# Optimization experiments

Measured on AMD Instinct MI355X. Metric: run time of the kernel, lower is better.

## Reference

```python
import jax, jax.numpy as jnp
import numpy as np

B, TQ, TI, TT = 8, 256, 256, 256
H, NH, F, E = 1024, 16, 4096, 8
HD = H // NH
EPS = 1e-5


def _ln(x, g, b):
    m = x.mean(-1, keepdims=True)
    v = ((x - m) ** 2).mean(-1, keepdims=True)
    return (x - m) / jnp.sqrt(v + EPS) * g + b


def _mha(q, k, v, in_w, in_b, out_w, out_b):
    # torch nn.MultiheadAttention: packed in_proj [3H,H], out_proj [H,H]
    wq, wk, wv = jnp.split(in_w, 3, axis=0)
    bq, bk, bv = jnp.split(in_b, 3, axis=0)
    Bq, Tq, _ = q.shape
    Tk = k.shape[1]
    qh = (q @ wq.T + bq).reshape(Bq, Tq, NH, HD)
    kh = (k @ wk.T + bk).reshape(Bq, Tk, NH, HD)
    vh = (v @ wv.T + bv).reshape(Bq, Tk, NH, HD)
    scores = jnp.einsum('bqhd,bkhd->bhqk', qh, kh) / jnp.sqrt(jnp.float32(HD))
    attn = jax.nn.softmax(scores, axis=-1)
    out = jnp.einsum('bhqk,bkhd->bqhd', attn, vh).reshape(Bq, Tq, H)
    return out @ out_w.T + out_b


def _moe(x, w1, b1, w2, b2, probs):
    # dense all-expert FFN: GELU(x W1 + b1) W2 + b2, mixed by router probs
    h = jax.nn.gelu(jnp.einsum('bth,ehf->btef', x, w1) + b1, approximate=False)
    o = jnp.einsum('btef,efh->bteh', h, w2) + b2
    return (o * probs[..., None]).sum(axis=-2)


def setup_inputs() -> dict:
    key = jax.random.key(0)
    ks = jax.random.split(key, 24)
    s = 0.02
    d = {}
    d['query_tokens'] = jax.random.normal(ks[0], (B, TQ, H), jnp.float32)
    d['image_tokens'] = jax.random.normal(ks[1], (B, TI, H), jnp.float32)
    d['text_context'] = jax.random.normal(ks[2], (B, TT, H), jnp.float32)
    d['sa_in_w'] = jax.random.normal(ks[3], (3 * H, H), jnp.float32) * s
    d['sa_in_b'] = jnp.zeros((3 * H,), jnp.float32)
    d['sa_out_w'] = jax.random.normal(ks[4], (H, H), jnp.float32) * s
    d['sa_out_b'] = jnp.zeros((H,), jnp.float32)
    d['ca_in_w'] = jax.random.normal(ks[5], (3 * H, H), jnp.float32) * s
    d['ca_in_b'] = jnp.zeros((3 * H,), jnp.float32)
    d['ca_out_w'] = jax.random.normal(ks[6], (H, H), jnp.float32) * s
    d['ca_out_b'] = jnp.zeros((H,), jnp.float32)
    d['img_gate_w'] = jax.random.normal(ks[7], (E, 2 * H), jnp.float32) * s
    d['img_gate_b'] = jnp.zeros((E,), jnp.float32)
    d['txt_gate_w'] = jax.random.normal(ks[8], (E, 2 * H), jnp.float32) * s
    d['txt_gate_b'] = jnp.zeros((E,), jnp.float32)
    d['lnq_g'] = jnp.ones((H,), jnp.float32)
    d['lnq_b'] = jnp.zeros((H,), jnp.float32)
    d['lnc_g'] = jnp.ones((H,), jnp.float32)
    d['lnc_b'] = jnp.zeros((H,), jnp.float32)
    d['lnf_g'] = jnp.ones((H,), jnp.float32)
    d['lnf_b'] = jnp.zeros((H,), jnp.float32)
    d['ew1'] = jax.random.normal(ks[9], (E, H, F), jnp.float32) * s
    d['eb1'] = jnp.zeros((E, F), jnp.float32)
    d['ew2'] = jax.random.normal(ks[10], (E, F, H), jnp.float32) * s
    d['eb2'] = jnp.zeros((E, H), jnp.float32)
    return d


def reference(query_tokens, image_tokens, text_context,
              sa_in_w, sa_in_b, sa_out_w, sa_out_b,
              ca_in_w, ca_in_b, ca_out_w, ca_out_b,
              img_gate_w, img_gate_b, txt_gate_w, txt_gate_b,
              lnq_g, lnq_b, lnc_g, lnc_b, lnf_g, lnf_b,
              ew1, eb1, ew2, eb2):
    # self-attention on query stream (dropout is identity in eval)
    q_norm = _ln(query_tokens, lnq_g, lnq_b)
    query_tokens = query_tokens + _mha(q_norm, q_norm, q_norm, sa_in_w, sa_in_b, sa_out_w, sa_out_b)
    # cross-attention query -> image tokens
    cross_norm = _ln(query_tokens, lnc_g, lnc_b)
    query_tokens = query_tokens + _mha(cross_norm, image_tokens, image_tokens, ca_in_w, ca_in_b, ca_out_w, ca_out_b)
    # gating contexts
    image_ctx = image_tokens.mean(axis=1, keepdims=True)   # [B,1,H]
    text_ctx = text_context.mean(axis=1, keepdims=True)    # [B,1,H]
    img_gate_in = jnp.concatenate([image_tokens, jnp.broadcast_to(text_ctx, image_tokens.shape)], axis=-1)
    txt_gate_in = jnp.concatenate([query_tokens, jnp.broadcast_to(image_ctx, query_tokens.shape)], axis=-1)
    temp = jnp.maximum(jnp.float32(1.0), 0.001)  # router temperature buffer = 1.0
    image_probs = jax.nn.softmax((img_gate_in @ img_gate_w.T + img_gate_b) / temp, axis=-1)
    text_probs = jax.nn.softmax((txt_gate_in @ txt_gate_w.T + txt_gate_b) / temp, axis=-1)
    # dense MoE (ep_group is None -> all experts evaluated, mixed by full softmax)
    q_ffn = _ln(query_tokens, lnf_g, lnf_b)
    query_tokens = query_tokens + _moe(q_ffn, ew1, eb1, ew2, eb2, text_probs)
    image_tokens = image_tokens + _moe(image_tokens, ew1, eb1, ew2, eb2, image_probs)
    return query_tokens, image_tokens
```

## Files before the change

### kernel.cpp

```cpp
#include <hip/hip_runtime.h>
#include <math.h>

typedef unsigned short u16;
typedef __bf16 bf16x8 __attribute__((ext_vector_type(8)));
typedef float  f32x4  __attribute__((ext_vector_type(4)));
typedef unsigned short u16x8 __attribute__((ext_vector_type(8)));
typedef unsigned short u16x4 __attribute__((ext_vector_type(4)));

union B8 { u16x8 u; bf16x8 b; };

__device__ __forceinline__ u16 f2bf(float x) {
  unsigned int u = __float_as_uint(x);
  unsigned int r = (u + 0x7fffu + ((u >> 16) & 1u)) >> 16;
  return (u16)r;
}
__device__ __forceinline__ float bf2f(u16 h) {
  return __uint_as_float(((unsigned int)h) << 16);
}

__device__ __forceinline__ void gload16(const void* g, void* l) {
  __builtin_amdgcn_global_load_lds(
      (const __attribute__((address_space(1))) unsigned int*)g,
      (__attribute__((address_space(3))) unsigned int*)l, 16, 0, 0);
}

__global__ __launch_bounds__(256) void cast_kernel(const float* __restrict__ in,
                                                   u16* __restrict__ out, int n4) {
  int i = blockIdx.x * 256 + threadIdx.x;
  if (i >= n4) return;
  f32x4 v = *(const f32x4*)(in + (size_t)i * 4);
  u16x4 o;
  o[0] = f2bf(v[0]); o[1] = f2bf(v[1]); o[2] = f2bf(v[2]); o[3] = f2bf(v[3]);
  *(u16x4*)(out + (size_t)i * 4) = o;
}

__global__ void transpose_cast_kernel(const float* __restrict__ in, u16* __restrict__ out,
                                      int R, int C) {
  __shared__ float tile[32][33];
  int z = blockIdx.z;
  int r0 = blockIdx.y * 32, c0 = blockIdx.x * 32;
  const float* ip = in + (size_t)z * R * C;
  u16* op = out + (size_t)z * R * C;
  int tx = threadIdx.x, ty = threadIdx.y;
  #pragma unroll
  for (int i = 0; i < 32; i += 8)
    tile[ty + i][tx] = ip[(size_t)(r0 + ty + i) * C + c0 + tx];
  __syncthreads();
  #pragma unroll
  for (int i = 0; i < 32; i += 8)
    op[(size_t)(c0 + ty + i) * R + r0 + tx] = f2bf(tile[tx][ty + i]);
}

__global__ __launch_bounds__(256) void ln_kernel(const float* __restrict__ in,
                                                 const float* __restrict__ g,
                                                 const float* __restrict__ bt,
                                                 u16* __restrict__ out) {
  __shared__ float red[4];
  int row = blockIdx.x;
  int t = threadIdx.x;
  int lane = t & 63, wid = t >> 6;
  f32x4 x = *(const f32x4*)(in + (size_t)row * 1024 + t * 4);
  float s = x[0] + x[1] + x[2] + x[3];
  #pragma unroll
  for (int o = 32; o > 0; o >>= 1) s += __shfl_down(s, o, 64);
  if (lane == 0) red[wid] = s;
  __syncthreads();
  float mean = (red[0] + red[1] + red[2] + red[3]) * (1.0f / 1024.0f);
  __syncthreads();
  float d0 = x[0] - mean, d1 = x[1] - mean, d2 = x[2] - mean, d3 = x[3] - mean;
  float s2 = d0 * d0 + d1 * d1 + d2 * d2 + d3 * d3;
  #pragma unroll
  for (int o = 32; o > 0; o >>= 1) s2 += __shfl_down(s2, o, 64);
  if (lane == 0) red[wid] = s2;
  __syncthreads();
  float var = (red[0] + red[1] + red[2] + red[3]) * (1.0f / 1024.0f);
  float rstd = rsqrtf(var + 1e-5f);
  f32x4 gg = *(const f32x4*)(g + t * 4);
  f32x4 bb = *(const f32x4*)(bt + t * 4);
  u16x4 o;
  o[0] = f2bf(d0 * rstd * gg[0] + bb[0]);
  o[1] = f2bf(d1 * rstd * gg[1] + bb[1]);
  o[2] = f2bf(d2 * rstd * gg[2] + bb[2]);
  o[3] = f2bf(d3 * rstd * gg[3] + bb[3]);
  *(u16x4*)(out + (size_t)row * 1024 + t * 4) = o;
}

__device__ __forceinline__ float gelu_f(float x) {
  float y = 0.79788456080286536f * (x + 0.044715f * x * x * x);
  return x - __fdividef(x, __expf(2.0f * y) + 1.0f);
}

#define SRC_COL(t) ((((t) & 3) ^ (((t) >> 3) & 3)) * 8)

template <int MODE, int ZB, int CHUNK>
__global__ __launch_bounds__(256, 3) void gemm_bt(const u16* __restrict__ A,
                                                  const u16* __restrict__ B,
                                                  const float* __restrict__ bias,
                                                  const float* __restrict__ extra,
                                                  void* __restrict__ out,
                                                  int M, int N, int K, int expertBase,
                                                  int kChunk, size_t saz, size_t sbz,
                                                  int sbiasz, size_t soutz) {
  __shared__ u16 sm[24576];
  const int tid = threadIdx.x;
  const int lane = tid & 63;
  const int wid = tid >> 6;
  const int wr = wid >> 1, wc = wid & 1;
  const int l15 = lane & 15;
  const int kg = lane >> 4;
  const int kgr8 = (kg ^ ((lane >> 1) & 3)) * 8;
  const int z = blockIdx.z;

  if (ZB) { A += (size_t)z * saz; B += (size_t)z * sbz; bias += z * sbiasz; }
  const int kOff = ZB ? 0 : z * kChunk;
  const bool z0 = ZB ? true : (z == 0);
  const int expert = expertBase + (ZB ? z : 0);

  const int gx = gridDim.x, gy = gridDim.y;
  const int bid = blockIdx.y * gx + blockIdx.x;
  const int xcd = bid & 7;
  const int idx = bid >> 3;
  int m0, n0;
  if constexpr (CHUNK == 0) {
    const int nwg = gx * gy;
    const int swz = xcd * (nwg >> 3) + idx;
    m0 = (swz / gx) * 128;
    n0 = (swz % gx) * 128;
  } else {
    const int hy = gy >> 2, hx = gx >> 1;
    const int cy = xcd >> 1, cx = xcd & 1;
    m0 = (cy * hy + idx % hy) * 128;
    n0 = (cx * hx + idx / hy) * 128;
  }

  f32x4 acc[4][4];
  #pragma unroll
  for (int i = 0; i < 4; i++)
    #pragma unroll
    for (int j = 0; j < 4; j++) acc[i][j] = f32x4{0.f, 0.f, 0.f, 0.f};

  const int sc = SRC_COL(tid);
  const u16* ga = A + (size_t)(m0 + (tid >> 2)) * K + sc + kOff;
  const u16* gb = B + (size_t)(n0 + (tid >> 2)) * K + sc + kOff;
  const size_t rowskip = (size_t)64 * K;

#define STG(b, kt)                                                  \
  do {                                                              \
    u16* d = sm + (b) * 8192 + wid * 512;                           \
    gload16(ga + (kt), d);                                          \
    gload16(ga + rowskip + (kt), d + 2048);                         \
    gload16(gb + (kt), d + 4096);                                   \
    gload16(gb + rowskip + (kt), d + 6144);                         \
  } while (0)

  const int NT = kChunk >> 5;
  STG(0, 0); STG(1, 32);
  int buf = 0;
  for (int t = 0; t < NT; ++t) {
    if (t + 1 < NT) asm volatile("s_waitcnt vmcnt(4)" ::: "memory");
    else            asm volatile("s_waitcnt vmcnt(0)" ::: "memory");
    __builtin_amdgcn_s_barrier();
    if (t + 2 < NT) {
      int nb = buf + 2; if (nb >= 3) nb -= 3;
      STG(nb, (t + 2) * 32);
    }
    __builtin_amdgcn_sched_barrier(0);
    __builtin_amdgcn_s_setprio(1);
    const u16* base = sm + buf * 8192;
    B8 af[4], bfr[4];
    #pragma unroll
    for (int i = 0; i < 4; i++) {
      af[i].u  = *(const u16x8*)(base + (wr * 64 + l15 + i * 16) * 32 + kgr8);
      bfr[i].u = *(const u16x8*)(base + 4096 + (wc * 64 + l15 + i * 16) * 32 + kgr8);
    }
    #pragma unroll
    for (int i = 0; i < 4; i++)
      #pragma unroll
      for (int j = 0; j < 4; j++)
        acc[i][j] = __builtin_amdgcn_mfma_f32_16x16x32_bf16(af[i].b, bfr[j].b, acc[i][j], 0, 0, 0);
    __builtin_amdgcn_s_setprio(0);
    if (++buf >= 3) buf = 0;
  }
#undef STG

  const int orow0 = m0 + wr * 64 + (lane >> 4) * 4;
  const int ocol0 = n0 + wc * 64 + l15;

  if constexpr (MODE == 0 || MODE == 2) {
    u16* outp = (u16*)out + (ZB ? (size_t)z * soutz : 0);
    __builtin_amdgcn_s_barrier();
    u16* rp = sm + wid * 1152;
    const int mrow0 = m0 + wr * 64;
    const int cbase = n0 + wc * 64;
    #pragma unroll
    for (int i = 0; i < 4; i++) {
      #pragma unroll
      for (int j = 0; j < 4; j++) {
        const float bb = bias[cbase + j * 16 + l15];
        #pragma unroll
        for (int p = 0; p < 4; p++) {
          float vb = acc[i][j][p] + bb;
          if constexpr (MODE == 2) vb = gelu_f(vb);
          rp[((lane >> 4) * 4 + p) * 72 + j * 16 + l15] = f2bf(vb);
        }
      }
      asm volatile("s_waitcnt lgkmcnt(0)" ::: "memory");
      #pragma unroll
      for (int rr = 0; rr < 4; rr++) {
        const int r16 = rr * 4 + (lane >> 4);
        u16x4 v4 = *(const u16x4*)&rp[r16 * 72 + l15 * 4];
        *(u16x4*)(outp + (size_t)(mrow0 + i * 16 + r16) * N + cbase + l15 * 4) = v4;
      }
      asm volatile("s_waitcnt lgkmcnt(0)" ::: "memory");
    }
  } else {
    float* outp = (float*)out + (ZB ? (size_t)z * soutz : 0);
    #pragma unroll
    for (int i = 0; i < 4; i++) {
      float pr_[4];
      if constexpr (MODE == 3) {
        #pragma unroll
        for (int p = 0; p < 4; p++)
          pr_[p] = extra[(size_t)(orow0 + i * 16 + p) * 8 + expert];
      }
      #pragma unroll
      for (int j = 0; j < 4; j++) {
        const int gcol = ocol0 + j * 16;
        const float bb = bias[gcol];
        #pragma unroll
        for (int p = 0; p < 4; p++) {
          const int grow = orow0 + i * 16 + p;
          const size_t off = (size_t)grow * N + gcol;
          if constexpr (MODE == 1) {
            atomicAdd(&outp[off], acc[i][j][p] + (z0 ? bb + extra[off] : 0.f));
          } else {
            atomicAdd(&outp[off], pr_[p] * (acc[i][j][p] + bb));
          }
        }
      }
    }
  }
}

__global__ __launch_bounds__(512, 2) void gemm8p(const u16* __restrict__ A,
                                                 const u16* __restrict__ B,
                                                 const float* __restrict__ bias,
                                                 u16* __restrict__ out,
                                                 int N, int K,
                                                 size_t sbz, int sbiasz, size_t soutz) {
  __shared__ u16 sm[65536];
  const int tid = threadIdx.x;
  const int lane = tid & 63;
  const int wid = tid >> 6;
  const int wr = wid >> 2;
  const int wc = wid & 3;
  const int l15 = lane & 15;
  const int kg = lane >> 4;
  const int kgr8 = (kg ^ ((lane >> 1) & 3)) * 8;
  const int z = blockIdx.z;
  B += (size_t)z * sbz; bias += z * sbiasz;
  u16* outp = out + (size_t)z * soutz;

  const int gx = gridDim.x, gy = gridDim.y;
  const int bid = blockIdx.y * gx + blockIdx.x;
  const int xcd = bid & 7;
  const int idx = bid >> 3;
  const int hy = gy >> 2, hx = gx >> 1;
  const int cy = xcd >> 1, cx = xcd & 1;
  const int m0 = (cy * hy + idx % hy) * 256;
  const int n0 = (cx * hx + idx / hy) * 256;

  f32x4 acc[8][4];
  #pragma unroll
  for (int i = 0; i < 8; i++)
    #pragma unroll
    for (int j = 0; j < 4; j++) acc[i][j] = f32x4{0.f, 0.f, 0.f, 0.f};

  const int sc = SRC_COL(tid);
  const u16* gaA0 = A + (size_t)(m0 + (tid >> 2)) * K + sc;
  const u16* gaA1 = A + (size_t)(m0 + 128 + (tid >> 2)) * K + sc;
  const u16* gbB0 = B + (size_t)(n0 + (tid >> 2)) * K + sc;
  const u16* gbB1 = B + (size_t)(n0 + 128 + (tid >> 2)) * K + sc;

#define STG_A(sp)                                                   \
  do {                                                              \
    u16* d = sm + ((sp) & 3) * 8192 + wid * 512;                    \
    gload16(gaA0 + (size_t)(sp) * 32, d);                           \
    gload16(gaA1 + (size_t)(sp) * 32, d + 4096);                    \
  } while (0)
#define STG_B(sp)                                                   \
  do {                                                              \
    u16* d = sm + 32768 + ((sp) & 3) * 8192 + wid * 512;            \
    gload16(gbB0 + (size_t)(sp) * 32, d);                           \
    gload16(gbB1 + (size_t)(sp) * 32, d + 4096);                    \
  } while (0)

  const int NT = K >> 5;
  STG_A(0); STG_B(0); STG_A(1); STG_B(1); STG_A(2); STG_B(2);
  asm volatile("s_waitcnt vmcnt(8)" ::: "memory");
  __builtin_amdgcn_s_barrier();

  for (int s = 0; s < NT; ++s) {
    const u16* bA = sm + (s & 3) * 8192;
    const u16* bB = sm + 32768 + (s & 3) * 8192;
    B8 bfr[4], af[4];
    #pragma unroll
    for (int j = 0; j < 4; j++)
      bfr[j].u = *(const u16x8*)(bB + (wc * 64 + j * 16 + l15) * 32 + kgr8);
    #pragma unroll
    for (int i = 0; i < 4; i++)
      af[i].u = *(const u16x8*)(bA + (wr * 128 + i * 16 + l15) * 32 + kgr8);
    if (s + 3 < NT) STG_A(s + 3);
    __builtin_amdgcn_s_barrier();
    asm volatile("s_waitcnt lgkmcnt(0)" ::: "memory");
    __builtin_amdgcn_sched_barrier(0);
    __builtin_amdgcn_s_setprio(1);
    #pragma unroll
    for (int i = 0; i < 4; i++)
      #pragma unroll
      for (int j = 0; j < 4; j++)
        acc[i][j] = __builtin_amdgcn_mfma_f32_16x16x32_bf16(af[i].b, bfr[j].b, acc[i][j], 0, 0, 0);
    __builtin_amdgcn_s_setprio(0);
    __builtin_amdgcn_s_barrier();
    B8 af2[4];
    #pragma unroll
    for (int i = 0; i < 4; i++)
      af2[i].u = *(const u16x8*)(bA + (wr * 128 + (i + 4) * 16 + l15) * 32 + kgr8);
    if (s + 3 < NT) STG_B(s + 3);
    __builtin_amdgcn_s_barrier();
    asm volatile("s_waitcnt lgkmcnt(0)" ::: "memory");
    __builtin_amdgcn_sched_barrier(0);
    __builtin_amdgcn_s_setprio(1);
    #pragma unroll
    for (int i = 0; i < 4; i++)
      #pragma unroll
      for (int j = 0; j < 4; j++)
        acc[i + 4][j] = __builtin_amdgcn_mfma_f32_16x16x32_bf16(af2[i].b, bfr[j].b, acc[i + 4][j], 0, 0, 0);
    __builtin_amdgcn_s_setprio(0);
    if (s + 3 < NT)      asm volatile("s_waitcnt vmcnt(8)" ::: "memory");
    else if (s + 2 < NT) asm volatile("s_waitcnt vmcnt(4)" ::: "memory");
    else                 asm volatile("s_waitcnt vmcnt(0)" ::: "memory");
    __builtin_amdgcn_s_barrier();
  }
#undef STG_A
#undef STG_B

  __builtin_amdgcn_s_barrier();
  u16* rp = sm + wid * 1152;
  const int mrow0 = m0 + wr * 128;
  const int cbase = n0 + wc * 64;
  #pragma unroll
  for (int i = 0; i < 8; i++) {
    #pragma unroll
    for (int j = 0; j < 4; j++) {
      const float bb = bias[cbase + j * 16 + l15];
      #pragma unroll
      for (int p = 0; p < 4; p++) {
        float vb = gelu_f(acc[i][j][p] + bb);
        rp[((lane >> 4) * 4 + p) * 72 + j * 16 + l15] = f2bf(vb);
      }
    }
    asm volatile("s_waitcnt lgkmcnt(0)" ::: "memory");
    #pragma unroll
    for (int rr = 0; rr < 4; rr++) {
      const int r16 = rr * 4 + (lane >> 4);
      u16x4 v4 = *(const u16x4*)&rp[r16 * 72 + l15 * 4];
      *(u16x4*)(outp + (size_t)(mrow0 + i * 16 + r16) * N + cbase + l15 * 4) = v4;
    }
    asm volatile("s_waitcnt lgkmcnt(0)" ::: "memory");
  }
}

__global__ __launch_bounds__(256) void attn_mfma(const u16* __restrict__ qb, int qs,
                                                 const u16* __restrict__ kb_, int ks,
                                                 const u16* __restrict__ vb, int vs,
                                                 u16* __restrict__ outp) {
  __shared__ u16 Ks[64][72];
  __shared__ u16 Vt[64][72];
  __shared__ u16 Pl[4][64][72];
  const int t = threadIdx.x;
  const int lane = t & 63;
  const int w = t >> 6;
  const int b = blockIdx.x >> 4;
  const int h = blockIdx.x & 15;
  const int lr = lane & 15;
  const int kg = lane >> 4;
  const size_t qrow0 = (size_t)b * 256 + w * 64;

  B8 qf[4][2];
  #pragma unroll
  for (int i = 0; i < 4; i++)
    #pragma unroll
    for (int kk = 0; kk < 2; kk++)
      qf[i][kk].u = *(const u16x8*)(qb + (qrow0 + i * 16 + lr) * qs + h * 64 + kk * 32 + kg * 8);

  f32x4 ao[4][4];
  float m_[4][4], l_[4][4];
  #pragma unroll
  for (int i = 0; i < 4; i++)
    #pragma unroll
    for (int n = 0; n < 4; n++) ao[i][n] = f32x4{0.f, 0.f, 0.f, 0.f};
  #pragma unroll
  for (int i = 0; i < 4; i++)
    #pragma unroll
    for (int p = 0; p < 4; p++) { m_[i][p] = -1e30f; l_[i][p] = 0.f; }

  for (int jt = 0; jt < 4; ++jt) {
    __syncthreads();
    {
      int r = t >> 2, c = (t & 3) * 16;
      const u16* src = kb_ + ((size_t)b * 256 + jt * 64 + r) * ks + h * 64 + c;
      *(u16x8*)&Ks[r][c] = *(const u16x8*)src;
      *(u16x8*)&Ks[r][c + 8] = *(const u16x8*)(src + 8);
      int jj = t & 63;
      const u16* vsrc = vb + ((size_t)b * 256 + jt * 64 + jj) * vs + h * 64 + w * 16;
      u16x8 v0 = *(const u16x8*)vsrc;
      u16x8 v1 = *(const u16x8*)(vsrc + 8);
      #pragma unroll
      for (int d = 0; d < 8; d++) Vt[w * 16 + d][jj] = v0[d];
      #pragma unroll
      for (int d = 0; d < 8; d++) Vt[w * 16 + 8 + d][jj] = v1[d];
    }
    __syncthreads();

    B8 kf[2][4];
    #pragma unroll
    for (int kk = 0; kk < 2; kk++)
      #pragma unroll
      for (int n = 0; n < 4; n++)
        kf[kk][n].u = *(const u16x8*)&Ks[n * 16 + lr][kk * 32 + kg * 8];

    #pragma unroll
    for (int i = 0; i < 4; i++) {
      f32x4 s[4];
      #pragma unroll
      for (int n = 0; n < 4; n++) s[n] = f32x4{0.f, 0.f, 0.f, 0.f};
      #pragma unroll
      for (int kk = 0; kk < 2; kk++)
        #pragma unroll
        for (int n = 0; n < 4; n++)
          s[n] = __builtin_amdgcn_mfma_f32_16x16x32_bf16(qf[i][kk].b, kf[kk][n].b, s[n], 0, 0, 0);
      #pragma unroll
      for (int p = 0; p < 4; p++) {
        float pm = fmaxf(fmaxf(s[0][p], s[1][p]), fmaxf(s[2][p], s[3][p])) * 0.125f;
        #pragma unroll
        for (int mk = 1; mk < 16; mk <<= 1) pm = fmaxf(pm, __shfl_xor(pm, mk, 16));
        float mn = fmaxf(m_[i][p], pm);
        float scl = __expf(m_[i][p] - mn);
        m_[i][p] = mn;
        float rs = 0.f;
        #pragma unroll
        for (int n = 0; n < 4; n++) {
          float e = __expf(s[n][p] * 0.125f - mn);
          Pl[w][i * 16 + kg * 4 + p][n * 16 + lr] = f2bf(e);
          rs += e;
        }
        #pragma unroll
        for (int mk = 1; mk < 16; mk <<= 1) rs += __shfl_xor(rs, mk, 16);
        l_[i][p] = l_[i][p] * scl + rs;
        #pragma unroll
        for (int n2 = 0; n2 < 4; n2++) ao[i][n2][p] *= scl;
      }
    }

    B8 vf[2][4];
    #pragma unroll
    for (int kk = 0; kk < 2; kk++)
      #pragma unroll
      for (int n2 = 0; n2 < 4; n2++)
        vf[kk][n2].u = *(const u16x8*)&Vt[n2 * 16 + lr][kk * 32 + kg * 8];
    #pragma unroll
    for (int i = 0; i < 4; i++) {
      #pragma unroll
      for (int kk = 0; kk < 2; kk++) {
        B8 pa;
        pa.u = *(const u16x8*)&Pl[w][i * 16 + lr][kk * 32 + kg * 8];
        #pragma unroll
        for (int n2 = 0; n2 < 4; n2++)
          ao[i][n2] = __builtin_amdgcn_mfma_f32_16x16x32_bf16(pa.b, vf[kk][n2].b, ao[i][n2], 0, 0, 0);
      }
    }
  }

  #pragma unroll
  for (int i = 0; i < 4; i++) {
    #pragma unroll
    for (int p = 0; p < 4; p++) {
      const float inv = 1.0f / l_[i][p];
      const size_t row = qrow0 + i * 16 + kg * 4 + p;
      #pragma unroll
      for (int n2 = 0; n2 < 4; n2++)
        outp[row * 1024 + h * 64 + n2 * 16 + lr] = f2bf(ao[i][n2][p] * inv);
    }
  }
}

__global__ __launch_bounds__(256) void mean2_kernel(const float* __restrict__ in,
                                                    float* __restrict__ out) {
  __shared__ float part[128];
  const int blk = blockIdx.x;
  const int b = blk >> 3, ch = blk & 7;
  const int t = threadIdx.x;
  const int col = ch * 128 + (t & 127);
  const int half = t >> 7;
  const float* p = in + (size_t)b * 262144 + (size_t)half * 131072 + col;
  float s = 0.f;
  for (int r = 0; r < 128; r++) s += p[(size_t)r * 1024];
  if (half) part[t & 127] = s;
  __syncthreads();
  if (!half) out[b * 1024 + col] = (s + part[t & 127]) * (1.0f / 256.0f);
}

__global__ __launch_bounds__(256) void gate_kernel(const float* __restrict__ x,
                                                   const float* __restrict__ ctx,
                                                   const float* __restrict__ gw,
                                                   const float* __restrict__ gb,
                                                   float* __restrict__ probs, int rowoff) {
  __shared__ float lg[8];
  const int tok = blockIdx.x;
  const int b = tok >> 8;
  const int t = threadIdx.x;
  const int e = t >> 5, sl = t & 31;
  const float* xr = x + (size_t)tok * 1024;
  const float* cr = ctx + (size_t)b * 1024;
  const float* wrow = gw + (size_t)e * 2048;
  float s = 0.f;
  for (int c = sl; c < 1024; c += 32) s += xr[c] * wrow[c] + cr[c] * wrow[1024 + c];
  #pragma unroll
  for (int o = 16; o > 0; o >>= 1) s += __shfl_down(s, o, 32);
  if (sl == 0) lg[e] = s + gb[e];
  __syncthreads();
  if (t == 0) {
    float mx = lg[0];
    #pragma unroll
    for (int i = 1; i < 8; i++) mx = fmaxf(mx, lg[i]);
    float ex[8], sum = 0.f;
    #pragma unroll
    for (int i = 0; i < 8; i++) { ex[i] = expf(lg[i] - mx); sum += ex[i]; }
    float inv = 1.0f / sum;
    #pragma unroll
    for (int i = 0; i < 8; i++) probs[(size_t)(rowoff + tok) * 8 + i] = ex[i] * inv;
  }
}

__global__ __launch_bounds__(256) void final_add_kernel(const float* __restrict__ q3,
                                                        const float* __restrict__ img,
                                                        const float* __restrict__ moe,
                                                        float* __restrict__ out) {
  size_t i = (size_t)blockIdx.x * 256 + threadIdx.x;
  f32x4 m4 = *(const f32x4*)(moe + i * 4);
  f32x4 a4 = (i < 524288) ? *(const f32x4*)(q3 + i * 4)
                          : *(const f32x4*)(img + (i - 524288) * 4);
  f32x4 r;
  r[0] = a4[0] + m4[0]; r[1] = a4[1] + m4[1]; r[2] = a4[2] + m4[2]; r[3] = a4[3] + m4[3];
  *(f32x4*)(out + i * 4) = r;
}

extern "C" void kernel_launch(void* const* d_in, const int* in_sizes, int n_in,
                              void* d_out, int out_size, void* d_ws, size_t ws_size,
                              hipStream_t stream) {
  const float* query_in = (const float*)d_in[0];
  const float* image_in = (const float*)d_in[1];
  const float* text_in  = (const float*)d_in[2];
  const float* sa_in_w  = (const float*)d_in[3];
  const float* sa_in_b  = (const float*)d_in[4];
  const float* sa_out_w = (const float*)d_in[5];
  const float* sa_out_b = (const float*)d_in[6];
  const float* ca_in_w  = (const float*)d_in[7];
  const float* ca_in_b  = (const float*)d_in[8];
  const float* ca_out_w = (const float*)d_in[9];
  const float* ca_out_b = (const float*)d_in[10];
  const float* img_gate_w = (const float*)d_in[11];
  const float* img_gate_b = (const float*)d_in[12];
  const float* txt_gate_w = (const float*)d_in[13];
  const float* txt_gate_b = (const float*)d_in[14];
  const float* lnq_g = (const float*)d_in[15];
  const float* lnq_b = (const float*)d_in[16];
  const float* lnc_g = (const float*)d_in[17];
  const float* lnc_b = (const float*)d_in[18];
  const float* lnf_g = (const float*)d_in[19];
  const float* lnf_b = (const float*)d_in[20];
  const float* ew1 = (const float*)d_in[21];
  const float* eb1 = (const float*)d_in[22];
  const float* ew2 = (const float*)d_in[23];
  const float* eb2 = (const float*)d_in[24];

  char* base = (char*)d_ws;
  size_t off = 0;
  auto alloc = [&](size_t bytes) -> char* {
    char* p = base + off;
    off += (bytes + 255) & ~(size_t)255;
    return p;
  };

  u16* wsa_in  = (u16*)alloc((size_t)3072 * 1024 * 2);
  u16* wsa_out = (u16*)alloc((size_t)1024 * 1024 * 2);
  u16* wca_in  = (u16*)alloc((size_t)3072 * 1024 * 2);
  u16* wca_out = (u16*)alloc((size_t)1024 * 1024 * 2);
  u16* w1T = (u16*)alloc((size_t)8 * 4096 * 1024 * 2);
  u16* w2T = (u16*)alloc((size_t)8 * 4096 * 1024 * 2);
  char* big = alloc((size_t)67108864);
  float* q3 = (float*)alloc((size_t)2048 * 1024 * 4);
  u16* xmoe = (u16*)alloc((size_t)4096 * 1024 * 2);
  float* moeac = (float*)alloc((size_t)4096 * 1024 * 4);
  float* probs = (float*)alloc((size_t)4096 * 8 * 4);
  float* ctx = (float*)alloc((size_t)2 * 8192 * 4);

  u16* qn      = (u16*)big;
  u16* qkv     = (u16*)(big + 4194304);
  u16* attn_o  = (u16*)(big + 16777216);
  float* q2    = (float*)(big + 20971520);
  u16* cnorm   = (u16*)(big + 29360128);
  u16* qca     = (u16*)(big + 33554432);
  u16* kvca    = (u16*)(big + 37748736);
  u16* h1p     = (u16*)big;
  u16* img_bf  = xmoe + (size_t)2048 * 1024;

  cast_kernel<<<3072, 256, 0, stream>>>(sa_in_w, wsa_in, 786432);
  cast_kernel<<<1024, 256, 0, stream>>>(sa_out_w, wsa_out, 262144);
  cast_kernel<<<3072, 256, 0, stream>>>(ca_in_w, wca_in, 786432);
  cast_kernel<<<1024, 256, 0, stream>>>(ca_out_w, wca_out, 262144);
  transpose_cast_kernel<<<dim3(128, 32, 8), dim3(32, 8), 0, stream>>>(ew1, w1T, 1024, 4096);
  transpose_cast_kernel<<<dim3(32, 128, 8), dim3(32, 8), 0, stream>>>(ew2, w2T, 4096, 1024);
  cast_kernel<<<2048, 256, 0, stream>>>(image_in, img_bf, 524288);

  ln_kernel<<<2048, 256, 0, stream>>>(query_in, lnq_g, lnq_b, qn);
  gemm_bt<0, 0, 0><<<dim3(24, 16), 256, 0, stream>>>(qn, wsa_in, sa_in_b, nullptr, qkv,
                                                     2048, 3072, 1024, 0, 1024, 0, 0, 0, 0);
  attn_mfma<<<128, 256, 0, stream>>>(qkv, 3072, qkv + 1024, 3072, qkv + 2048, 3072, attn_o);
  hipMemsetAsync(q2, 0, (size_t)2048 * 1024 * 4, stream);
  gemm_bt<1, 0, 0><<<dim3(8, 16, 2), 256, 0, stream>>>(attn_o, wsa_out, sa_out_b, query_in, q2,
                                                       2048, 1024, 1024, 0, 512, 0, 0, 0, 0);

  ln_kernel<<<2048, 256, 0, stream>>>(q2, lnc_g, lnc_b, cnorm);
  gemm_bt<0, 0, 0><<<dim3(8, 16), 256, 0, stream>>>(cnorm, wca_in, ca_in_b, nullptr, qca,
                                                    2048, 1024, 1024, 0, 1024, 0, 0, 0, 0);
  gemm_bt<0, 0, 0><<<dim3(16, 16), 256, 0, stream>>>(img_bf, wca_in + (size_t)1024 * 1024,
                                                     ca_in_b + 1024, nullptr, kvca,
                                                     2048, 2048, 1024, 0, 1024, 0, 0, 0, 0);
  attn_mfma<<<128, 256, 0, stream>>>(qca, 1024, kvca, 2048, kvca + 1024, 2048, attn_o);
  hipMemsetAsync(q3, 0, (size_t)2048 * 1024 * 4, stream);
  gemm_bt<1, 0, 0><<<dim3(8, 16, 2), 256, 0, stream>>>(attn_o, wca_out, ca_out_b, q2, q3,
                                                       2048, 1024, 1024, 0, 512, 0, 0, 0, 0);

  mean2_kernel<<<64, 256, 0, stream>>>(image_in, ctx);
  mean2_kernel<<<64, 256, 0, stream>>>(text_in, ctx + 8192);
  gate_kernel<<<2048, 256, 0, stream>>>(q3, ctx, txt_gate_w, txt_gate_b, probs, 0);
  gate_kernel<<<2048, 256, 0, stream>>>(image_in, ctx + 8192, img_gate_w, img_gate_b, probs, 2048);

  ln_kernel<<<2048, 256, 0, stream>>>(q3, lnf_g, lnf_b, xmoe);
  hipMemsetAsync(moeac, 0, (size_t)4096 * 1024 * 4, stream);
  for (int e0 = 0; e0 < 8; e0 += 2) {
    gemm8p<<<dim3(16, 16, 2), 512, 0, stream>>>(
        xmoe, w1T + (size_t)e0 * 4194304, eb1 + (size_t)e0 * 4096, h1p,
        4096, 1024,  4194304,  4096,  16777216);
    gemm_bt<3, 1, 0><<<dim3(8, 32, 2), 256, 0, stream>>>(
        h1p, w2T + (size_t)e0 * 4194304, eb2 + (size_t)e0 * 1024, probs, moeac,
        4096, 1024, 4096, e0, 4096,
         16777216,  4194304,  1024,  0);
  }

  final_add_kernel<<<4096, 256, 0, stream>>>(q3, image_in, moeac, (float*)d_out);
}
```

Baseline: 1.125 ms.

## Use 256x256 gemm8p tile with split-K for MoE down-projection

Generalizes the 8-wave 256x256-tile gemm8p kernel with a mode template, a split-K option and a probability-weighted atomic-add epilogue. The MoE second GEMM (h1 times W2) now runs on it, replacing gemm_bt, with K split in two halves per expert. The aim is to get the larger tile's data reuse and deeper pipeline for the down-projection while keeping enough blocks via split-K. In exchange, every output element takes one more atomic add.

```diff
diff --git a/kernel.cpp b/kernel.cpp
--- a/kernel.cpp
+++ b/kernel.cpp
@@ -242,12 +242,15 @@
   }
 }
 
+template <int MODE, int SPLITK>
 __global__ __launch_bounds__(512, 2) void gemm8p(const u16* __restrict__ A,
                                                  const u16* __restrict__ B,
                                                  const float* __restrict__ bias,
-                                                 u16* __restrict__ out,
-                                                 int N, int K,
-                                                 size_t sbz, int sbiasz, size_t soutz) {
+                                                 const float* __restrict__ extra,
+                                                 void* __restrict__ out,
+                                                 int N, int K, int kChunk, int expertBase,
+                                                 size_t saz, size_t sbz, int sbiasz,
+                                                 size_t soutz) {
   __shared__ u16 sm[65536];
   const int tid = threadIdx.x;
   const int lane = tid & 63;
@@ -258,8 +261,12 @@
   const int kg = lane >> 4;
   const int kgr8 = (kg ^ ((lane >> 1) & 3)) * 8;
   const int z = blockIdx.z;
-  B += (size_t)z * sbz; bias += z * sbiasz;
-  u16* outp = out + (size_t)z * soutz;
+  const int ze = SPLITK ? (z >> 1) : z;
+  const int kh = SPLITK ? (z & 1) : 0;
+  A += (size_t)ze * saz; B += (size_t)ze * sbz; bias += ze * sbiasz;
+  const int kOff = kh * kChunk;
+  const bool kh0 = (kh == 0);
+  const int expert = expertBase + ze;
 
   const int gx = gridDim.x, gy = gridDim.y;
   const int bid = blockIdx.y * gx + blockIdx.x;
@@ -277,10 +284,10 @@
     for (int j = 0; j < 4; j++) acc[i][j] = f32x4{0.f, 0.f, 0.f, 0.f};
 
   const int sc = SRC_COL(tid);
-  const u16* gaA0 = A + (size_t)(m0 + (tid >> 2)) * K + sc;
-  const u16* gaA1 = A + (size_t)(m0 + 128 + (tid >> 2)) * K + sc;
-  const u16* gbB0 = B + (size_t)(n0 + (tid >> 2)) * K + sc;
-  const u16* gbB1 = B + (size_t)(n0 + 128 + (tid >> 2)) * K + sc;
+  const u16* gaA0 = A + (size_t)(m0 + (tid >> 2)) * K + sc + kOff;
+  const u16* gaA1 = A + (size_t)(m0 + 128 + (tid >> 2)) * K + sc + kOff;
+  const u16* gbB0 = B + (size_t)(n0 + (tid >> 2)) * K + sc + kOff;
+  const u16* gbB1 = B + (size_t)(n0 + 128 + (tid >> 2)) * K + sc + kOff;
 
 #define STG_A(sp)                                                   \
   do {                                                              \
@@ -295,7 +302,7 @@
     gload16(gbB1 + (size_t)(sp) * 32, d + 4096);                    \
   } while (0)
 
-  const int NT = K >> 5;
+  const int NT = kChunk >> 5;
   STG_A(0); STG_B(0); STG_A(1); STG_B(1); STG_A(2); STG_B(2);
   asm volatile("s_waitcnt vmcnt(8)" ::: "memory");
   __builtin_amdgcn_s_barrier();
@@ -345,29 +352,54 @@
 #undef STG_A
 #undef STG_B
 
-  __builtin_amdgcn_s_barrier();
-  u16* rp = sm + wid * 1152;
-  const int mrow0 = m0 + wr * 128;
-  const int cbase = n0 + wc * 64;
-  #pragma unroll
-  for (int i = 0; i < 8; i++) {
-    #pragma unroll
-    for (int j = 0; j < 4; j++) {
-      const float bb = bias[cbase + j * 16 + l15];
-      #pragma unroll
-      for (int p = 0; p < 4; p++) {
-        float vb = gelu_f(acc[i][j][p] + bb);
-        rp[((lane >> 4) * 4 + p) * 72 + j * 16 + l15] = f2bf(vb);
-      }
-    }
-    asm volatile("s_waitcnt lgkmcnt(0)" ::: "memory");
-    #pragma unroll
-    for (int rr = 0; rr < 4; rr++) {
-      const int r16 = rr * 4 + (lane >> 4);
-      u16x4 v4 = *(const u16x4*)&rp[r16 * 72 + l15 * 4];
-      *(u16x4*)(outp + (size_t)(mrow0 + i * 16 + r16) * N + cbase + l15 * 4) = v4;
-    }
-    asm volatile("s_waitcnt lgkmcnt(0)" ::: "memory");
+  if constexpr (MODE == 2) {
+    u16* outp = (u16*)out + (size_t)ze * soutz;
+    __builtin_amdgcn_s_barrier();
+    u16* rp = sm + wid * 1152;
+    const int mrow0 = m0 + wr * 128;
+    const int cbase = n0 + wc * 64;
+    #pragma unroll
+    for (int i = 0; i < 8; i++) {
+      #pragma unroll
+      for (int j = 0; j < 4; j++) {
+        const float bb = bias[cbase + j * 16 + l15];
+        #pragma unroll
+        for (int p = 0; p < 4; p++) {
+          float vb = gelu_f(acc[i][j][p] + bb);
+          rp[((lane >> 4) * 4 + p) * 72 + j * 16 + l15] = f2bf(vb);
+        }
+      }
+      asm volatile("s_waitcnt lgkmcnt(0)" ::: "memory");
+      #pragma unroll
+      for (int rr = 0; rr < 4; rr++) {
+        const int r16 = rr * 4 + (lane >> 4);
+        u16x4 v4 = *(const u16x4*)&rp[r16 * 72 + l15 * 4];
+        *(u16x4*)(outp + (size_t)(mrow0 + i * 16 + r16) * N + cbase + l15 * 4) = v4;
+      }
+      asm volatile("s_waitcnt lgkmcnt(0)" ::: "memory");
+    }
+  } else {
+    float* outp = (float*)out;
+    const int orow0 = m0 + wr * 128 + (lane >> 4) * 4;
+    const int ocol0 = n0 + wc * 64 + l15;
+    #pragma unroll
+    for (int i = 0; i < 8; i++) {
+      float pr_[4];
+      #pragma unroll
+      for (int p = 0; p < 4; p++)
+        pr_[p] = extra[(size_t)(orow0 + i * 16 + p) * 8 + expert];
+      #pragma unroll
+      for (int j = 0; j < 4; j++) {
+        const int gcol = ocol0 + j * 16;
+        const float bb = bias[gcol];
+        #pragma unroll
+        for (int p = 0; p < 4; p++) {
+          const int grow = orow0 + i * 16 + p;
+          const size_t off = (size_t)grow * N + gcol;
+          atomicAdd(&outp[off], pr_[p] * (acc[i][j][p] + (kh0 ? bb : 0.f)));
+        }
+      }
+    }
   }
 }
 
@@ -651,12 +683,13 @@
   ln_kernel<<<2048, 256, 0, stream>>>(q3, lnf_g, lnf_b, xmoe);
   hipMemsetAsync(moeac, 0, (size_t)4096 * 1024 * 4, stream);
   for (int e0 = 0; e0 < 8; e0 += 2) {
-    gemm8p<<<dim3(16, 16, 2), 512, 0, stream>>>(
-        xmoe, w1T + (size_t)e0 * 4194304, eb1 + (size_t)e0 * 4096, h1p,
-        4096, 1024,  4194304,  4096,  16777216);
-    gemm_bt<3, 1, 0><<<dim3(8, 32, 2), 256, 0, stream>>>(
+    gemm8p<2, 0><<<dim3(16, 16, 2), 512, 0, stream>>>(
+        xmoe, w1T + (size_t)e0 * 4194304, eb1 + (size_t)e0 * 4096, nullptr, h1p,
+        4096, 1024, 1024, e0,
+         0,  4194304,  4096,  16777216);
+    gemm8p<3, 1><<<dim3(4, 16, 4), 512, 0, stream>>>(
         h1p, w2T + (size_t)e0 * 4194304, eb2 + (size_t)e0 * 1024, probs, moeac,
-        4096, 1024, 4096, e0, 4096,
+        1024, 4096, 2048, e0,
          16777216,  4194304,  1024,  0);
   }
 
```

Result: slower. 1.153 ms (+2.4%).
